# Kernel optimization log

Hardware: AMD Instinct MI355X
Metric: run time of the kernel (lower is better)

## Reference

```python
import jax, jax.numpy as jnp
import numpy as np

B, L, D, H, V = 4, 128, 128, 8, 32000
N_ITER = 4
DAMP_H = DAMP_Z = DAMP_X = 0.0
STEP_H = STEP_Z = STEP_X = 1.0
REG_H = REG_Z = REG_X = 1.0
BLOCK_MSG = False
NEG = 1e9


def _norm(t):
    # norm='softmax'
    return jax.nn.softmax(t, axis=-1)


def setup_inputs() -> dict:
    key = jax.random.key(0)
    k1, k2, k3, k4 = jax.random.split(key, 4)
    x = jax.random.normal(k1, (B, L, D), dtype=jnp.float32)
    mask = jnp.ones((B, L), dtype=jnp.int32)
    m_mask = jax.random.randint(k2, (B, L), 0, 2).astype(jnp.int32)
    embed_matrix = jax.random.normal(k3, (V, D), dtype=jnp.float32)
    ternary = jax.random.normal(k4, (2, D, D, H), dtype=jnp.float32)  # dists='' -> 2 groups
    return {"x": x, "mask": mask, "embed_matrix": embed_matrix, "m_mask": m_mask, "ternary": ternary}


def _forward(x, mask, embed_matrix, m_mask, ternary):
    dt = x.dtype
    mask1d = mask != 0                                   # [B,L] True = real token
    valid2d = mask1d[:, :, None] & mask1d[:, None, :]    # [B,L,L]
    inv2d = ~valid2d[:, None, :, :]                      # broadcast over heads
    keep = mask1d[..., None].astype(dt)                  # [B,L,1]
    mm = m_mask.astype(dt)[..., None]                    # [B,L,1]

    # distance mask: dists='' -> [triu(1); tril(-1)] -> [2,L,L]
    dm = jnp.triu(jnp.ones((L, L), dt), 1)
    distmask = jnp.stack([dm, dm.T], axis=0)

    eye = jnp.eye(L, dtype=dt)

    unary = x
    q_x = jnp.ones((B, L, V), dt)
    # initialize_Z=True: masked positions start from expected embedding
    pre = _norm(q_x) @ embed_matrix                      # [B,L,D]
    q_z = unary * (1.0 - mm) + pre * mm
    q_z = q_z * keep

    q_h = jnp.ones((B, H, L, L), dt) - eye * NEG
    q_h = jnp.where(inv2d, -NEG, q_h)

    cache_qh, cache_qz, cache_qx = q_h, q_z, q_x
    # async_update=True: normalize Z before first H update
    q_z = _norm(q_z) * keep

    for _ in range(N_ITER):
        # ---- H update: F[z,c,i,j] = sum_{k,a,b} q_z[z,i,a] q_z[z,j,b] T[k,a,b,c] dist[k,i,j]
        t1 = jnp.einsum('zia,kabc->zkibc', q_z, ternary)            # [B,2,L,D,H]
        F = jnp.einsum('zkibc,zjb,kij->zcij', t1, q_z, distmask)    # [B,H,L,L]
        q_h = cache_qh * DAMP_H + F * (1.0 - DAMP_H) / REG_H
        q_h = cache_qh * (1.0 - STEP_H) + q_h * STEP_H
        cache_qh = q_h
        q_h = q_h - eye * NEG
        q_h = jnp.where(inv2d, -NEG, q_h)
        q_hn = _norm(q_h)                                           # [B,H,L,L]

        # ---- Z update: first-order messages from ternary factors
        m = q_hn[:, None] * distmask[None, :, None]                 # [B,2,H,L,L]
        s1 = jnp.einsum('zkcij,zjb->zkibc', m, q_z)                 # to Z_i (head slot)
        G = jnp.einsum('zkibc,kabc->zia', s1, ternary)
        if not BLOCK_MSG:
            s2 = jnp.einsum('zkcij,zia->zkjac', m, q_z)             # to Z_j (dep slot)
            G = G + jnp.einsum('zkjac,kabc->zjb', s2, ternary)

        # unary: X message replaces word unary at <MASK> positions
        unary_eff = unary * (1.0 - mm) + (_norm(q_x) @ embed_matrix) * mm
        q_z_new = cache_qz * DAMP_Z + (unary_eff + G) * (1.0 - DAMP_Z) / REG_Z
        q_z_new = cache_qz * (1.0 - STEP_Z) + q_z_new * STEP_Z
        cache_qz = q_z_new
        q_z = _norm(q_z_new) * keep

        # ---- X update: message from Z through embedding factor
        msg_x = jnp.einsum('zia,va->ziv', q_z, embed_matrix)        # [B,L,V]
        q_x_new = cache_qx * DAMP_X + msg_x * (1.0 - DAMP_X) / REG_X
        q_x_new = cache_qx * (1.0 - STEP_X) + q_x_new * STEP_X
        cache_qx = q_x_new
        q_x = q_x_new

    # output_prob=False -> unnormalized scores
    return q_x


def reference(x, mask, embed_matrix, m_mask, ternary):
    return _forward(x, mask, embed_matrix, m_mask, ternary)
```

## Files before the change

### kernel.cpp

```cpp
#include <hip/hip_runtime.h>
#include <math.h>

#define L_ 128
#define D_ 128
#define H_ 8
#define V_ 32000
#define NEGC 1e9f

typedef short short8 __attribute__((ext_vector_type(8)));
typedef float f32x4 __attribute__((ext_vector_type(4)));
typedef unsigned short ushort8v __attribute__((ext_vector_type(8)));

__device__ __forceinline__ unsigned short f2bf(float x) {
    unsigned int u = __float_as_uint(x);
    unsigned int r = (u + 0x7fff + ((u >> 16) & 1)) >> 16;
    return (unsigned short)r;
}


__global__ __launch_bounds__(256) void prep_k(const float* __restrict__ E,
                                              unsigned short* __restrict__ Ebf,
                                              unsigned short* __restrict__ Etf,
                                              const float* __restrict__ T, float* __restrict__ Tt,
                                              const int* __restrict__ m_mask,
                                              int* __restrict__ rowidx, int* __restrict__ nactb,
                                              float* __restrict__ meansum) {
    __shared__ __align__(16) unsigned char psmem[8704];
    int blk = blockIdx.x;
    int t = threadIdx.x;
    if (blk < 1000) {
        unsigned short* tile = (unsigned short*)psmem;
        int v0 = blk * 32;
#pragma unroll
        for (int i = 0; i < 4; ++i) {
            int idx = i * 256 + t;
            int v = idx >> 5;
            int d4 = (idx & 31) * 4;
            float4 val = *(const float4*)&E[(size_t)(v0 + v) * 128 + d4];
            tile[v * 136 + d4 + 0] = f2bf(val.x);
            tile[v * 136 + d4 + 1] = f2bf(val.y);
            tile[v * 136 + d4 + 2] = f2bf(val.z);
            tile[v * 136 + d4 + 3] = f2bf(val.w);
        }
        __syncthreads();
        {
            int fi = t >> 5;
            int l0 = (t & 31) * 2;
            int vtl = fi >> 2, s = fi & 3;
            size_t base = ((size_t)(blk * 2 + vtl) * 4 + s) * 512;
#pragma unroll
            for (int li = 0; li < 2; ++li) {
                int l = l0 + li;
                int nl = l & 15, hf = l >> 4;
                ushort8v o;
#pragma unroll
                for (int j = 0; j < 8; ++j) o[j] = tile[(vtl * 16 + nl) * 136 + s * 32 + hf * 8 + j];
                *(ushort8v*)&Ebf[base + l * 8] = o;
            }
        }
        {
            int ct = t >> 5;
            int l0 = (t & 31) * 2;
            size_t base = ((size_t)blk * 8 + ct) * 512;
#pragma unroll
            for (int li = 0; li < 2; ++li) {
                int l = l0 + li;
                int nl = l & 15, hf = l >> 4;
                ushort8v o;
#pragma unroll
                for (int j = 0; j < 8; ++j) o[j] = tile[(hf * 8 + j) * 136 + ct * 16 + nl];
                *(ushort8v*)&Etf[base + l * 8] = o;
            }
        }
    } else if (blk < 1256) {
        int tb = blk - 1000;
        for (int q = 0; q < 4; ++q) {
            int id = tb * 1024 + q * 256 + t;
            int k = id >> 17;
            int rem = id & 131071;
            int a = rem >> 10;
            int bc = rem & 1023;
            int b = bc >> 3, c = bc & 7;
            Tt[k * 131072 + b * 1024 + a * 8 + c] = T[id];
        }
    } else if (blk == 1256) {
        int* wc = (int*)psmem;
        bool a0 = m_mask[t] != 0;
        bool a1 = m_mask[t + 256] != 0;
        unsigned long long b0 = __ballot(a0);
        unsigned long long b1 = __ballot(a1);
        int w = t >> 6, lane = t & 63;
        if (lane == 0) { wc[w] = __popcll(b0); wc[4 + w] = __popcll(b1); }
        __syncthreads();
        int base0 = 0;
        for (int i = 0; i < w; ++i) base0 += wc[i];
        int base1 = 0;
        for (int i = 0; i < 4 + w; ++i) base1 += wc[i];
        if (a0) rowidx[base0 + __popcll(b0 & ((1ull << lane) - 1))] = t;
        if (a1) rowidx[base1 + __popcll(b1 & ((1ull << lane) - 1))] = t + 256;
        if (t == 0) {
            int tot = 0;
            for (int i = 0; i < 8; ++i) tot += wc[i];
            nactb[0] = tot;
        }
    } else {
        float* red = (float*)psmem;
        int d = t & 127, h = t >> 7;
        int v0 = (blk - 1257) * 256;
        float s = 0.f;
        for (int p = 0; p < 128; ++p)
            s += E[(size_t)(v0 + h + 2 * p) * 128 + d];
        red[t] = s;
        __syncthreads();
        if (h == 0) atomicAdd(&meansum[d], red[d] + red[128 + d]);
    }
}

__global__ __launch_bounds__(64) void init_k(const float* __restrict__ x, const int* __restrict__ mask,
                                             const int* __restrict__ m_mask, const float* __restrict__ meansum,
                                             float* __restrict__ ue, float* __restrict__ qz,
                                             unsigned short* __restrict__ qzb) {
    int row = blockIdx.x, t = threadIdx.x;
    float keepv = mask[row] ? 1.f : 0.f;
    bool mm = m_mask[row] != 0;
    float pre0 = meansum[t] * (1.f / 32000.f);
    float pre1 = meansum[t + 64] * (1.f / 32000.f);
    float u0 = mm ? pre0 : x[row * 128 + t];
    float u1 = mm ? pre1 : x[row * 128 + t + 64];
    ue[row * 128 + t] = u0;
    ue[row * 128 + t + 64] = u1;
    float sv0 = u0 * keepv, sv1 = u1 * keepv;
    float m = fmaxf(sv0, sv1);
    for (int off = 32; off; off >>= 1) m = fmaxf(m, __shfl_xor(m, off));
    float e0 = __expf(sv0 - m), e1 = __expf(sv1 - m);
    float s = e0 + e1;
    for (int off = 32; off; off >>= 1) s += __shfl_xor(s, off);
    float inv = keepv / s;
    float q0 = e0 * inv, q1 = e1 * inv;
    qz[row * 128 + t] = q0;
    qz[row * 128 + t + 64] = q1;
    qzb[row * 128 + t] = f2bf(q0);
    qzb[row * 128 + t + 64] = f2bf(q1);
}


__global__ __launch_bounds__(256) void fusedA_k(const float* __restrict__ qz, const float* __restrict__ T,
                                                const float* __restrict__ Tt, float* __restrict__ U2,
                                                unsigned short* __restrict__ Ut, unsigned short* __restrict__ Wt,
                                                const unsigned short* __restrict__ qzb,
                                                const unsigned short* __restrict__ Ebf,
                                                const unsigned short* __restrict__ Etf,
                                                const int* __restrict__ rowidx, const int* __restrict__ nactb,
                                                float* __restrict__ partial, float* __restrict__ partial_rs) {
    __shared__ __align__(16) unsigned char smem[42752];
    int blk = blockIdx.x;
    int t = threadIdx.x;
    if (blk < 512) {
        float* aL = (float*)smem;
        int by = blk >> 5;
        int uw = by >> 3, z = (by >> 1) & 3, k = by & 1;
        int bx = blk & 31;
        int m0 = (bx >> 2) * 16, n = (bx & 3) * 256 + t;
        const float* A = qz + z * 16384;
        const float* Bm = (uw ? Tt : T) + k * 131072;
        for (int idx = t; idx < 2048; idx += 256)
            aL[idx] = A[(m0 + (idx >> 7)) * 128 + (idx & 127)];
        __syncthreads();
        float acc[16];
#pragma unroll
        for (int m = 0; m < 16; ++m) acc[m] = 0.f;
        for (int kq = 0; kq < 32; ++kq) {
            float b0 = Bm[(kq * 4 + 0) * 1024 + n];
            float b1 = Bm[(kq * 4 + 1) * 1024 + n];
            float b2 = Bm[(kq * 4 + 2) * 1024 + n];
            float b3 = Bm[(kq * 4 + 3) * 1024 + n];
#pragma unroll
            for (int m = 0; m < 16; ++m) {
                const float4 aq = *(const float4*)&aL[m * 128 + kq * 4];
                acc[m] += aq.x * b0 + aq.y * b1 + aq.z * b2 + aq.w * b3;
            }
        }
        if (uw == 0) {
            float* Cm = U2 + (z * 2 + k) * 131072;
#pragma unroll
            for (int m = 0; m < 16; ++m)
                Cm[(m0 + m) * 1024 + n] = acc[m];
        }
        int bb = n >> 3, cc = n & 7;
        ushort8v p0, p1;
#pragma unroll
        for (int m = 0; m < 8; ++m) { p0[m] = f2bf(acc[m]); p1[m] = f2bf(acc[8 + m]); }
        unsigned short* To = (uw ? Wt : Ut) + ((size_t)(z * 2 + k) * 128 + bb) * 1024 + cc * 128 + m0;
        *(ushort8v*)&To[0] = p0;
        *(ushort8v*)&To[8] = p1;
    } else {
        int nact = nactb[0];
        int bid = blk - 512;
        int xcd = bid & 7, idx = bid >> 3;
        int g = xcd + 8 * (idx >> 5);
        int bx = idx & 31;
        int r0 = bx * 16;
        if (g >= 50 || r0 >= nact) return;
        unsigned short* Pl = (unsigned short*)smem;
        float* slab = (float*)(smem + 9216);
        float* rsW  = (float*)(smem + 9216 + 33280);
        int w = t >> 6, lane = t & 63;
        int nloc = lane & 15, half = lane >> 4;
        int rA = r0 + nloc;
        bool actA = rA < nact;
        int rowA = actA ? rowidx[rA] : 0;
        short8 zero8 = (short8){0, 0, 0, 0, 0, 0, 0, 0};
        short8 afr[4];
#pragma unroll
        for (int s = 0; s < 4; ++s) {
            short8 v = *(const short8*)&qzb[rowA * 128 + s * 32 + half * 8];
            afr[s] = actA ? v : zero8;
        }
        const int kc0 = g * 20 + w * 5;
        short8 ebb[2][8];
#pragma unroll
        for (int f = 0; f < 8; ++f)
            ebb[0][f] = *(const short8*)&Ebf[((size_t)(kc0 * 8 + f)) * 512 + lane * 8];
        f32x4 acc2[8];
#pragma unroll
        for (int ct = 0; ct < 8; ++ct) acc2[ct] = (f32x4){0.f, 0.f, 0.f, 0.f};
        float rsl = 0.f;
#pragma unroll
        for (int step = 0; step < 5; ++step) {
            const int p = step & 1;
            const int kc = kc0 + step;
            short8 et[8];
#pragma unroll
            for (int f = 0; f < 8; ++f)
                et[f] = *(const short8*)&Etf[((size_t)(kc * 8 + f)) * 512 + lane * 8];
            if (step < 4) {
#pragma unroll
                for (int f = 0; f < 8; ++f)
                    ebb[p ^ 1][f] = *(const short8*)&Ebf[((size_t)((kc + 1) * 8 + f)) * 512 + lane * 8];
            }
            f32x4 p0 = (f32x4){0.f, 0.f, 0.f, 0.f};
            f32x4 p1 = (f32x4){0.f, 0.f, 0.f, 0.f};
#pragma unroll
            for (int s = 0; s < 4; ++s) {
                p0 = __builtin_amdgcn_mfma_f32_16x16x32_bf16(ebb[p][s], afr[s], p0, 0, 0, 0);
                p1 = __builtin_amdgcn_mfma_f32_16x16x32_bf16(ebb[p][4 + s], afr[s], p1, 0, 0, 0);
            }
            unsigned short* pw = Pl + (w * 2 + p) * 576;
            {
                float e0 = __expf(p0[0]), e1 = __expf(p0[1]), e2 = __expf(p0[2]), e3 = __expf(p0[3]);
                rsl += (e0 + e1) + (e2 + e3);
                uint2 pk = {(unsigned)f2bf(e0) | ((unsigned)f2bf(e1) << 16),
                            (unsigned)f2bf(e2) | ((unsigned)f2bf(e3) << 16)};
                *(uint2*)&pw[nloc * 36 + half * 4] = pk;
            }
            {
                float e0 = __expf(p1[0]), e1 = __expf(p1[1]), e2 = __expf(p1[2]), e3 = __expf(p1[3]);
                rsl += (e0 + e1) + (e2 + e3);
                uint2 pk = {(unsigned)f2bf(e0) | ((unsigned)f2bf(e1) << 16),
                            (unsigned)f2bf(e2) | ((unsigned)f2bf(e3) << 16)};
                *(uint2*)&pw[nloc * 36 + 16 + half * 4] = pk;
            }
            short8 a2 = *(const short8*)&pw[nloc * 36 + half * 8];
#pragma unroll
            for (int ct = 0; ct < 8; ++ct)
                acc2[ct] = __builtin_amdgcn_mfma_f32_16x16x32_bf16(a2, et[ct], acc2[ct], 0, 0, 0);
        }
        rsl += __shfl_xor(rsl, 16);
        rsl += __shfl_xor(rsl, 32);
        if (lane < 16) rsW[w * 16 + nloc] = rsl;
#pragma unroll
        for (int ct = 0; ct < 8; ++ct)
#pragma unroll
            for (int reg = 0; reg < 4; ++reg)
                slab[w * 2080 + (half * 4 + reg) * 130 + ct * 16 + nloc] = acc2[ct][reg];
        __syncthreads();
        float* pb = partial + (size_t)g * 65536;
        for (int i = t; i < 2048; i += 256) {
            int row = i >> 7, col = i & 127;
            int rr = r0 + row;
            if (rr < nact)
                pb[rr * 128 + col] = slab[row * 130 + col] + slab[2080 + row * 130 + col]
                                   + slab[4160 + row * 130 + col] + slab[6240 + row * 130 + col];
        }
        if (t < 16) {
            int rr = r0 + t;
            if (rr < nact)
                partial_rs[g * 512 + rr] = rsW[t] + rsW[16 + t] + rsW[32 + t] + rsW[48 + t];
        }
    }
}

__global__ __launch_bounds__(256) void fusedB_k(const float* __restrict__ qz, const float* __restrict__ U2,
                                                const int* __restrict__ mask,
                                                unsigned short* __restrict__ A0b, unsigned short* __restrict__ A1b,
                                                unsigned short* __restrict__ A0Tb, unsigned short* __restrict__ A1Tb,
                                                const float* __restrict__ partial, const float* __restrict__ partial_rs,
                                                const int* __restrict__ rowidx, const int* __restrict__ nactb,
                                                float* __restrict__ exbuf, float* __restrict__ rowsum) {
    __shared__ __align__(16) unsigned char smem[23552];
    int blk = blockIdx.x;
    int t = threadIdx.x;
    if (blk >= 256) {
        int nact = nactb[0];
        int idx = (blk - 256) * 256 + t;
        int rr = idx >> 7, col = idx & 127;
        if (rr >= nact) return;
        float s = 0.f;
#pragma unroll 10
        for (int g = 0; g < 50; ++g)
            s += partial[(size_t)g * 65536 + rr * 128 + col];
        int row = rowidx[rr];
        exbuf[row * 128 + col] = s;
        if (col == 0) {
            float ts = 0.f;
#pragma unroll 10
            for (int g = 0; g < 50; ++g) ts += partial_rs[g * 512 + rr];
            rowsum[row] = ts;
        }
        return;
    }
    float* As = (float*)smem;
    float* Bs = (float*)(smem + 4608);
    int* maskL = (int*)(smem + 4608 + 18432);
    int z = blk >> 6, c = (blk >> 3) & 7, iq = blk & 7;
    int i0 = iq * 16;
    int tj = t & 15, ti = t >> 4;
    int i = i0 + ti;
    if (t < 128) maskL[t] = mask[z * 128 + t];
    float acc0[8], acc1[8];
#pragma unroll
    for (int jj = 0; jj < 8; ++jj) { acc0[jj] = 0.f; acc1[jj] = 0.f; }
    const float* U2z = U2 + (size_t)z * 262144;
    const float* qzz = qz + z * 16384;
    for (int kb = 0; kb < 4; ++kb) {
        int b0 = kb * 32;
        __syncthreads();
        for (int e = t; e < 1024; e += 256) {
            int k = e >> 9, r = e & 511, ii = r >> 5, b = r & 31;
            As[(k * 16 + ii) * 36 + b] = U2z[k * 131072 + (i0 + ii) * 1024 + (b0 + b) * 8 + c];
        }
        for (int f = t; f < 1024; f += 256) {
            int j = f >> 3, b4 = f & 7;
            int slot = b4 ^ ((j >> 3) & 7);
            *(float4*)&Bs[j * 36 + slot * 4] = *(const float4*)&qzz[j * 128 + b0 + b4 * 4];
        }
        __syncthreads();
#pragma unroll
        for (int b4 = 0; b4 < 8; ++b4) {
            float4 a0 = *(const float4*)&As[(0 * 16 + ti) * 36 + b4 * 4];
            float4 a1 = *(const float4*)&As[(1 * 16 + ti) * 36 + b4 * 4];
#pragma unroll
            for (int jj = 0; jj < 8; ++jj) {
                int j = tj * 8 + jj;
                int slot = b4 ^ ((j >> 3) & 7);
                float4 bq = *(const float4*)&Bs[j * 36 + slot * 4];
                acc0[jj] += a0.x * bq.x;
                acc0[jj] += a0.y * bq.y;
                acc0[jj] += a0.z * bq.z;
                acc0[jj] += a0.w * bq.w;
                acc1[jj] += a1.x * bq.x;
                acc1[jj] += a1.y * bq.y;
                acc1[jj] += a1.z * bq.z;
                acc1[jj] += a1.w * bq.w;
            }
        }
    }
    bool vi = maskL[i] != 0;
    float fv[8];
#pragma unroll
    for (int jj = 0; jj < 8; ++jj) {
        int j2 = tj * 8 + jj;
        float F = (j2 > i) ? acc0[jj] : acc1[jj];
        if (j2 == i) F -= NEGC;
        if (!vi || maskL[j2] == 0) F = -NEGC;
        fv[jj] = F;
    }
    float mval = fv[0];
#pragma unroll
    for (int jj = 1; jj < 8; ++jj) mval = fmaxf(mval, fv[jj]);
    for (int off = 1; off < 16; off <<= 1) mval = fmaxf(mval, __shfl_xor(mval, off));
    float ssum = 0.f;
#pragma unroll
    for (int jj = 0; jj < 8; ++jj) ssum += __expf(fv[jj] - mval);
    for (int off = 1; off < 16; off <<= 1) ssum += __shfl_xor(ssum, off);
    float inv = 1.f / ssum;
    size_t base = (size_t)(z * 8 + c) * 16384;
    ushort8v v0, v1;
    unsigned short bvv[8];
#pragma unroll
    for (int jj = 0; jj < 8; ++jj) {
        int j2 = tj * 8 + jj;
        float val = __expf(fv[jj] - mval) * inv;
        unsigned short bv = f2bf(val);
        bvv[jj] = bv;
        v0[jj] = (j2 > i) ? bv : (unsigned short)0;
        v1[jj] = (j2 < i) ? bv : (unsigned short)0;
    }
    *(ushort8v*)&A0b[base + i * 128 + tj * 8] = v0;
    *(ushort8v*)&A1b[base + i * 128 + tj * 8] = v1;
#pragma unroll
    for (int jj = 0; jj < 8; ++jj) {
        int j2 = tj * 8 + jj;
        A0Tb[base + j2 * 128 + i] = (i < j2) ? bvv[jj] : (unsigned short)0;
        A1Tb[base + j2 * 128 + i] = (i > j2) ? bvv[jj] : (unsigned short)0;
    }
}

__global__ __launch_bounds__(64) void gkern_mfma_k(const unsigned short* __restrict__ A0b,
                                                   const unsigned short* __restrict__ A1b,
                                                   const unsigned short* __restrict__ A0Tb,
                                                   const unsigned short* __restrict__ A1Tb,
                                                   const unsigned short* __restrict__ Ut,
                                                   const unsigned short* __restrict__ Wt,
                                                   float* __restrict__ g1, float* __restrict__ g2) {
    int mode = blockIdx.y;
    int bx = blockIdx.x;
    int z = bx >> 6, it = (bx >> 3) & 7, at = bx & 7;
    int lane = threadIdx.x;
    int nloc = lane & 15, half = lane >> 4;
    int i0 = it * 16, a0 = at * 16;
    const unsigned short* Am0 = (mode ? A0Tb : A0b) + (size_t)z * 131072;
    const unsigned short* Am1 = (mode ? A1Tb : A1b) + (size_t)z * 131072;
    const unsigned short* Bt = mode ? Ut : Wt;
    const unsigned short* B0 = Bt + (size_t)(z * 2 + 0) * 131072 + (size_t)(a0 + nloc) * 1024;
    const unsigned short* B1 = Bt + (size_t)(z * 2 + 1) * 131072 + (size_t)(a0 + nloc) * 1024;
    const unsigned short* Ar0 = Am0 + (size_t)(i0 + nloc) * 128;
    const unsigned short* Ar1 = Am1 + (size_t)(i0 + nloc) * 128;
    f32x4 acc = (f32x4){0.f, 0.f, 0.f, 0.f};
#pragma unroll
    for (int c = 0; c < 8; ++c) {
#pragma unroll
        for (int sb = 0; sb < 4; ++sb) {
            int s0 = sb * 32 + half * 8;
            short8 av0 = *(const short8*)&Ar0[c * 16384 + s0];
            short8 bv0 = *(const short8*)&B0[c * 128 + s0];
            acc = __builtin_amdgcn_mfma_f32_16x16x32_bf16(av0, bv0, acc, 0, 0, 0);
            short8 av1 = *(const short8*)&Ar1[c * 16384 + s0];
            short8 bv1 = *(const short8*)&B1[c * 128 + s0];
            acc = __builtin_amdgcn_mfma_f32_16x16x32_bf16(av1, bv1, acc, 0, 0, 0);
        }
    }
    float* G = mode ? g2 : g1;
#pragma unroll
    for (int reg = 0; reg < 4; ++reg)
        G[(z * 128 + i0 + half * 4 + reg) * 128 + a0 + nloc] = acc[reg];
}

__global__ __launch_bounds__(64) void zupd_k(const float* __restrict__ ue, const float* __restrict__ x,
                                             const int* __restrict__ m_mask,
                                             const float* __restrict__ exbuf, const float* __restrict__ rowsum,
                                             const float* __restrict__ g1, const float* __restrict__ g2,
                                             const int* __restrict__ mask,
                                             float* __restrict__ qz, unsigned short* __restrict__ qzb, int useEx) {
    int row = blockIdx.x, t = threadIdx.x;
    float keepv = mask[row] ? 1.f : 0.f;
    int b = row * 128;
    float u0, u1;
    if (useEx) {
        if (m_mask[row] != 0) {
            float rsv = rowsum[row];
            u0 = exbuf[b + t] / rsv;
            u1 = exbuf[b + t + 64] / rsv;
        } else {
            u0 = x[b + t];
            u1 = x[b + t + 64];
        }
    } else {
        u0 = ue[b + t];
        u1 = ue[b + t + 64];
    }
    float v0 = u0 + g1[b + t] + g2[b + t];
    float v1 = u1 + g1[b + t + 64] + g2[b + t + 64];
    float m = fmaxf(v0, v1);
    for (int off = 32; off; off >>= 1) m = fmaxf(m, __shfl_xor(m, off));
    float e0 = __expf(v0 - m), e1 = __expf(v1 - m);
    float s = e0 + e1;
    for (int off = 32; off; off >>= 1) s += __shfl_xor(s, off);
    float inv = keepv / s;
    float q0 = e0 * inv, q1 = e1 * inv;
    qz[b + t] = q0;
    qz[b + t + 64] = q1;
    qzb[b + t] = f2bf(q0);
    qzb[b + t + 64] = f2bf(q1);
}

__global__ __launch_bounds__(256) void msgx_mfma_k(const unsigned short* __restrict__ qzb,
                                                   const unsigned short* __restrict__ Ebf,
                                                   float* __restrict__ out) {
    int t = threadIdx.x;
    int w = t >> 6, lane = t & 63;
    int nloc = lane & 15, half = lane >> 4;
    int rt0 = blockIdx.x * 64;
    int cb0 = blockIdx.y * 256 + w * 64;
    short8 afr[4][4];
#pragma unroll
    for (int r = 0; r < 4; ++r)
#pragma unroll
        for (int s = 0; s < 4; ++s)
            afr[r][s] = *(const short8*)&qzb[(rt0 + r * 16 + nloc) * 128 + s * 32 + half * 8];
    f32x4 acc[4][4];
#pragma unroll
    for (int r = 0; r < 4; ++r)
#pragma unroll
        for (int ct = 0; ct < 4; ++ct)
            acc[r][ct] = (f32x4){0.f, 0.f, 0.f, 0.f};
#pragma unroll
    for (int ct = 0; ct < 4; ++ct) {
#pragma unroll
        for (int s = 0; s < 4; ++s) {
            short8 bfr = *(const short8*)&Ebf[(((size_t)(cb0 >> 4) + ct) * 4 + s) * 512 + lane * 8];
#pragma unroll
            for (int r = 0; r < 4; ++r)
                acc[r][ct] = __builtin_amdgcn_mfma_f32_16x16x32_bf16(afr[r][s], bfr, acc[r][ct], 0, 0, 0);
        }
    }
#pragma unroll
    for (int r = 0; r < 4; ++r)
#pragma unroll
        for (int ct = 0; ct < 4; ++ct) {
            int col = cb0 + ct * 16 + nloc;
#pragma unroll
            for (int reg = 0; reg < 4; ++reg) {
                int row = rt0 + r * 16 + half * 4 + reg;
                out[(size_t)row * V_ + col] = acc[r][ct][reg];
            }
        }
}

extern "C" void kernel_launch(void* const* d_in, const int* in_sizes, int n_in,
                              void* d_out, int out_size, void* d_ws, size_t ws_size,
                              hipStream_t stream) {
    const float* x     = (const float*)d_in[0];
    const int*   mask  = (const int*)d_in[1];
    const float* E     = (const float*)d_in[2];
    const int*   mmask = (const int*)d_in[3];
    const float* T     = (const float*)d_in[4];
    float* out = (float*)d_out;

    float* w = (float*)d_ws;
    float* meansum = w;
    float* ue      = w + 128;
    float* qz      = ue + 65536;
    float* exbuf   = qz + 65536;
    float* rowsum  = exbuf + 65536;
    float* g1      = rowsum + 512;
    float* g2      = g1 + 65536;
    float* Tt      = g2 + 65536;
    float* U2      = Tt + 262144;
    float* prs     = U2 + 1048576;
    unsigned short* qzb  = (unsigned short*)(prs + 25600);
    unsigned short* Ebf  = qzb + 65536;
    unsigned short* Etf  = Ebf + 4096000;
    unsigned short* A0b  = Etf + 4096000;
    unsigned short* A1b  = A0b + 524288;
    unsigned short* A0Tb = A1b + 524288;
    unsigned short* A1Tb = A0Tb + 524288;
    unsigned short* Ut   = A1Tb + 524288;
    unsigned short* Wt   = Ut + 1048576;
    int* rowidx = (int*)(Wt + 1048576);
    int* nactb  = rowidx + 512;

    float* partial = out;

    hipMemsetAsync(meansum, 0, 128 * sizeof(float), stream);
    prep_k<<<1382, 256, 0, stream>>>(E, Ebf, Etf, T, Tt, mmask, rowidx, nactb, meansum);
    init_k<<<512, 64, 0, stream>>>(x, mask, mmask, meansum, ue, qz, qzb);

    for (int it = 0; it < 4; ++it) {
        fusedA_k<<<it ? 2304 : 512, 256, 0, stream>>>(qz, T, Tt, U2, Ut, Wt,
                                                      qzb, Ebf, Etf, rowidx, nactb, partial, prs);
        fusedB_k<<<it ? 512 : 256, 256, 0, stream>>>(qz, U2, mask, A0b, A1b, A0Tb, A1Tb,
                                                     partial, prs, rowidx, nactb, exbuf, rowsum);
        gkern_mfma_k<<<dim3(256, 2), 64, 0, stream>>>(A0b, A1b, A0Tb, A1Tb, Ut, Wt, g1, g2);
        zupd_k<<<512, 64, 0, stream>>>(ue, x, mmask, exbuf, rowsum, g1, g2, mask, qz, qzb, it ? 1 : 0);
    }
    msgx_mfma_k<<<dim3(8, 125), 256, 0, stream>>>(qzb, Ebf, out);
}
```

Before: 377.3 us.

## Fuse iteration loop into one persistent cooperative kernel with grid syncs

Replaces the 17 per-iteration kernel launches (four stages per iteration plus the final vocab projection) with one cooperative persistent kernel of 512 blocks. The blocks loop over the job lists and separate stages with grid.sync(). The goal is to remove launch overhead and inter-kernel gaps across the many small stages. In exchange, large stages such as the 2304-job pxe pass and the 1000-job msgx pass now run with a fixed 512-block grid, and each grid barrier has its own cost. A fallback path with separate launches remains for when the cooperative launch fails.

```diff
diff --git a/kernel.cpp b/kernel.cpp
--- a/kernel.cpp
+++ b/kernel.cpp
@@ -1,5 +1,8 @@
 #include <hip/hip_runtime.h>
+#include <hip/hip_cooperative_groups.h>
 #include <math.h>
+
+namespace cg = cooperative_groups;
 
 #define L_ 128
 #define D_ 128
@@ -16,6 +19,35 @@
     unsigned int r = (u + 0x7fff + ((u >> 16) & 1)) >> 16;
     return (unsigned short)r;
 }
+
+struct LoopArgs {
+    float* qz;
+    float* ue;
+    float* exbuf;
+    float* rowsum;
+    float* g1;
+    float* g2;
+    const float* x;
+    const float* T;
+    const float* Tt;
+    float* U2;
+    float* prs;
+    unsigned short* qzb;
+    const unsigned short* Ebf;
+    const unsigned short* Etf;
+    unsigned short* A0b;
+    unsigned short* A1b;
+    unsigned short* A0Tb;
+    unsigned short* A1Tb;
+    unsigned short* Ut;
+    unsigned short* Wt;
+    const int* mask;
+    const int* m_mask;
+    const int* rowidx;
+    const int* nactb;
+    float* partial;
+    float* out;
+};
 
 
 __global__ __launch_bounds__(256) void prep_k(const float* __restrict__ E,
@@ -144,181 +176,142 @@
 }
 
 
-__global__ __launch_bounds__(256) void fusedA_k(const float* __restrict__ qz, const float* __restrict__ T,
-                                                const float* __restrict__ Tt, float* __restrict__ U2,
-                                                unsigned short* __restrict__ Ut, unsigned short* __restrict__ Wt,
-                                                const unsigned short* __restrict__ qzb,
-                                                const unsigned short* __restrict__ Ebf,
-                                                const unsigned short* __restrict__ Etf,
-                                                const int* __restrict__ rowidx, const int* __restrict__ nactb,
-                                                float* __restrict__ partial, float* __restrict__ partial_rs) {
-    __shared__ __align__(16) unsigned char smem[42752];
-    int blk = blockIdx.x;
-    int t = threadIdx.x;
-    if (blk < 512) {
-        float* aL = (float*)smem;
-        int by = blk >> 5;
-        int uw = by >> 3, z = (by >> 1) & 3, k = by & 1;
-        int bx = blk & 31;
-        int m0 = (bx >> 2) * 16, n = (bx & 3) * 256 + t;
-        const float* A = qz + z * 16384;
-        const float* Bm = (uw ? Tt : T) + k * 131072;
-        for (int idx = t; idx < 2048; idx += 256)
-            aL[idx] = A[(m0 + (idx >> 7)) * 128 + (idx & 127)];
-        __syncthreads();
-        float acc[16];
-#pragma unroll
-        for (int m = 0; m < 16; ++m) acc[m] = 0.f;
-        for (int kq = 0; kq < 32; ++kq) {
-            float b0 = Bm[(kq * 4 + 0) * 1024 + n];
-            float b1 = Bm[(kq * 4 + 1) * 1024 + n];
-            float b2 = Bm[(kq * 4 + 2) * 1024 + n];
-            float b3 = Bm[(kq * 4 + 3) * 1024 + n];
-#pragma unroll
-            for (int m = 0; m < 16; ++m) {
-                const float4 aq = *(const float4*)&aL[m * 128 + kq * 4];
-                acc[m] += aq.x * b0 + aq.y * b1 + aq.z * b2 + aq.w * b3;
-            }
-        }
-        if (uw == 0) {
-            float* Cm = U2 + (z * 2 + k) * 131072;
-#pragma unroll
-            for (int m = 0; m < 16; ++m)
-                Cm[(m0 + m) * 1024 + n] = acc[m];
-        }
-        int bb = n >> 3, cc = n & 7;
-        ushort8v p0, p1;
-#pragma unroll
-        for (int m = 0; m < 8; ++m) { p0[m] = f2bf(acc[m]); p1[m] = f2bf(acc[8 + m]); }
-        unsigned short* To = (uw ? Wt : Ut) + ((size_t)(z * 2 + k) * 128 + bb) * 1024 + cc * 128 + m0;
-        *(ushort8v*)&To[0] = p0;
-        *(ushort8v*)&To[8] = p1;
-    } else {
-        int nact = nactb[0];
-        int bid = blk - 512;
-        int xcd = bid & 7, idx = bid >> 3;
-        int g = xcd + 8 * (idx >> 5);
-        int bx = idx & 31;
-        int r0 = bx * 16;
-        if (g >= 50 || r0 >= nact) return;
-        unsigned short* Pl = (unsigned short*)smem;
-        float* slab = (float*)(smem + 9216);
-        float* rsW  = (float*)(smem + 9216 + 33280);
-        int w = t >> 6, lane = t & 63;
-        int nloc = lane & 15, half = lane >> 4;
-        int rA = r0 + nloc;
-        bool actA = rA < nact;
-        int rowA = actA ? rowidx[rA] : 0;
-        short8 zero8 = (short8){0, 0, 0, 0, 0, 0, 0, 0};
-        short8 afr[4];
+__device__ __forceinline__ void dev_uwgemm(int blk, int t, unsigned char* smem, const LoopArgs& a) {
+    float* aL = (float*)smem;
+    int by = blk >> 5;
+    int uw = by >> 3, z = (by >> 1) & 3, k = by & 1;
+    int bx = blk & 31;
+    int m0 = (bx >> 2) * 16, n = (bx & 3) * 256 + t;
+    const float* A = a.qz + z * 16384;
+    const float* Bm = (uw ? a.Tt : a.T) + k * 131072;
+    for (int idx = t; idx < 2048; idx += 256)
+        aL[idx] = A[(m0 + (idx >> 7)) * 128 + (idx & 127)];
+    __syncthreads();
+    float acc[16];
+#pragma unroll
+    for (int m = 0; m < 16; ++m) acc[m] = 0.f;
+    for (int kq = 0; kq < 32; ++kq) {
+        float b0 = Bm[(kq * 4 + 0) * 1024 + n];
+        float b1 = Bm[(kq * 4 + 1) * 1024 + n];
+        float b2 = Bm[(kq * 4 + 2) * 1024 + n];
+        float b3 = Bm[(kq * 4 + 3) * 1024 + n];
+#pragma unroll
+        for (int m = 0; m < 16; ++m) {
+            const float4 aq = *(const float4*)&aL[m * 128 + kq * 4];
+            acc[m] += aq.x * b0 + aq.y * b1 + aq.z * b2 + aq.w * b3;
+        }
+    }
+    if (uw == 0) {
+        float* Cm = a.U2 + (z * 2 + k) * 131072;
+#pragma unroll
+        for (int m = 0; m < 16; ++m)
+            Cm[(m0 + m) * 1024 + n] = acc[m];
+    }
+    int bb = n >> 3, cc = n & 7;
+    ushort8v p0, p1;
+#pragma unroll
+    for (int m = 0; m < 8; ++m) { p0[m] = f2bf(acc[m]); p1[m] = f2bf(acc[8 + m]); }
+    unsigned short* To = (uw ? a.Wt : a.Ut) + ((size_t)(z * 2 + k) * 128 + bb) * 1024 + cc * 128 + m0;
+    *(ushort8v*)&To[0] = p0;
+    *(ushort8v*)&To[8] = p1;
+}
+
+__device__ __forceinline__ void dev_pxe(int bid, int t, unsigned char* smem, const LoopArgs& a) {
+    int nact = a.nactb[0];
+    int xcd = bid & 7, idx = bid >> 3;
+    int g = xcd + 8 * (idx >> 5);
+    int bx = idx & 31;
+    int r0 = bx * 16;
+    if (g >= 50 || r0 >= nact) return;
+    unsigned short* Pl = (unsigned short*)smem;
+    float* slab = (float*)(smem + 9216);
+    float* rsW  = (float*)(smem + 9216 + 33280);
+    int w = t >> 6, lane = t & 63;
+    int nloc = lane & 15, half = lane >> 4;
+    int rA = r0 + nloc;
+    bool actA = rA < nact;
+    int rowA = actA ? a.rowidx[rA] : 0;
+    short8 zero8 = (short8){0, 0, 0, 0, 0, 0, 0, 0};
+    short8 afr[4];
+#pragma unroll
+    for (int s = 0; s < 4; ++s) {
+        short8 v = *(const short8*)&a.qzb[rowA * 128 + s * 32 + half * 8];
+        afr[s] = actA ? v : zero8;
+    }
+    const int kc0 = g * 20 + w * 5;
+    short8 ebb[2][8];
+#pragma unroll
+    for (int f = 0; f < 8; ++f)
+        ebb[0][f] = *(const short8*)&a.Ebf[((size_t)(kc0 * 8 + f)) * 512 + lane * 8];
+    f32x4 acc2[8];
+#pragma unroll
+    for (int ct = 0; ct < 8; ++ct) acc2[ct] = (f32x4){0.f, 0.f, 0.f, 0.f};
+    float rsl = 0.f;
+#pragma unroll
+    for (int step = 0; step < 5; ++step) {
+        const int p = step & 1;
+        const int kc = kc0 + step;
+        short8 et[8];
+#pragma unroll
+        for (int f = 0; f < 8; ++f)
+            et[f] = *(const short8*)&a.Etf[((size_t)(kc * 8 + f)) * 512 + lane * 8];
+        if (step < 4) {
+#pragma unroll
+            for (int f = 0; f < 8; ++f)
+                ebb[p ^ 1][f] = *(const short8*)&a.Ebf[((size_t)((kc + 1) * 8 + f)) * 512 + lane * 8];
+        }
+        f32x4 p0 = (f32x4){0.f, 0.f, 0.f, 0.f};
+        f32x4 p1 = (f32x4){0.f, 0.f, 0.f, 0.f};
 #pragma unroll
         for (int s = 0; s < 4; ++s) {
-            short8 v = *(const short8*)&qzb[rowA * 128 + s * 32 + half * 8];
-            afr[s] = actA ? v : zero8;
-        }
-        const int kc0 = g * 20 + w * 5;
-        short8 ebb[2][8];
-#pragma unroll
-        for (int f = 0; f < 8; ++f)
-            ebb[0][f] = *(const short8*)&Ebf[((size_t)(kc0 * 8 + f)) * 512 + lane * 8];
-        f32x4 acc2[8];
-#pragma unroll
-        for (int ct = 0; ct < 8; ++ct) acc2[ct] = (f32x4){0.f, 0.f, 0.f, 0.f};
-        float rsl = 0.f;
-#pragma unroll
-        for (int step = 0; step < 5; ++step) {
-            const int p = step & 1;
-            const int kc = kc0 + step;
-            short8 et[8];
-#pragma unroll
-            for (int f = 0; f < 8; ++f)
-                et[f] = *(const short8*)&Etf[((size_t)(kc * 8 + f)) * 512 + lane * 8];
-            if (step < 4) {
-#pragma unroll
-                for (int f = 0; f < 8; ++f)
-                    ebb[p ^ 1][f] = *(const short8*)&Ebf[((size_t)((kc + 1) * 8 + f)) * 512 + lane * 8];
-            }
-            f32x4 p0 = (f32x4){0.f, 0.f, 0.f, 0.f};
-            f32x4 p1 = (f32x4){0.f, 0.f, 0.f, 0.f};
-#pragma unroll
-            for (int s = 0; s < 4; ++s) {
-                p0 = __builtin_amdgcn_mfma_f32_16x16x32_bf16(ebb[p][s], afr[s], p0, 0, 0, 0);
-                p1 = __builtin_amdgcn_mfma_f32_16x16x32_bf16(ebb[p][4 + s], afr[s], p1, 0, 0, 0);
-            }
-            unsigned short* pw = Pl + (w * 2 + p) * 576;
-            {
-                float e0 = __expf(p0[0]), e1 = __expf(p0[1]), e2 = __expf(p0[2]), e3 = __expf(p0[3]);
-                rsl += (e0 + e1) + (e2 + e3);
-                uint2 pk = {(unsigned)f2bf(e0) | ((unsigned)f2bf(e1) << 16),
-                            (unsigned)f2bf(e2) | ((unsigned)f2bf(e3) << 16)};
-                *(uint2*)&pw[nloc * 36 + half * 4] = pk;
-            }
-            {
-                float e0 = __expf(p1[0]), e1 = __expf(p1[1]), e2 = __expf(p1[2]), e3 = __expf(p1[3]);
-                rsl += (e0 + e1) + (e2 + e3);
-                uint2 pk = {(unsigned)f2bf(e0) | ((unsigned)f2bf(e1) << 16),
-                            (unsigned)f2bf(e2) | ((unsigned)f2bf(e3) << 16)};
-                *(uint2*)&pw[nloc * 36 + 16 + half * 4] = pk;
-            }
-            short8 a2 = *(const short8*)&pw[nloc * 36 + half * 8];
-#pragma unroll
-            for (int ct = 0; ct < 8; ++ct)
-                acc2[ct] = __builtin_amdgcn_mfma_f32_16x16x32_bf16(a2, et[ct], acc2[ct], 0, 0, 0);
-        }
-        rsl += __shfl_xor(rsl, 16);
-        rsl += __shfl_xor(rsl, 32);
-        if (lane < 16) rsW[w * 16 + nloc] = rsl;
+            p0 = __builtin_amdgcn_mfma_f32_16x16x32_bf16(ebb[p][s], afr[s], p0, 0, 0, 0);
+            p1 = __builtin_amdgcn_mfma_f32_16x16x32_bf16(ebb[p][4 + s], afr[s], p1, 0, 0, 0);
+        }
+        unsigned short* pw = Pl + (w * 2 + p) * 576;
+        {
+            float e0 = __expf(p0[0]), e1 = __expf(p0[1]), e2 = __expf(p0[2]), e3 = __expf(p0[3]);
+            rsl += (e0 + e1) + (e2 + e3);
+            uint2 pk = {(unsigned)f2bf(e0) | ((unsigned)f2bf(e1) << 16),
+                        (unsigned)f2bf(e2) | ((unsigned)f2bf(e3) << 16)};
+            *(uint2*)&pw[nloc * 36 + half * 4] = pk;
+        }
+        {
+            float e0 = __expf(p1[0]), e1 = __expf(p1[1]), e2 = __expf(p1[2]), e3 = __expf(p1[3]);
+            rsl += (e0 + e1) + (e2 + e3);
+            uint2 pk = {(unsigned)f2bf(e0) | ((unsigned)f2bf(e1) << 16),
+                        (unsigned)f2bf(e2) | ((unsigned)f2bf(e3) << 16)};
+            *(uint2*)&pw[nloc * 36 + 16 + half * 4] = pk;
+        }
+        short8 a2 = *(const short8*)&pw[nloc * 36 + half * 8];
 #pragma unroll
         for (int ct = 0; ct < 8; ++ct)
-#pragma unroll
-            for (int reg = 0; reg < 4; ++reg)
-                slab[w * 2080 + (half * 4 + reg) * 130 + ct * 16 + nloc] = acc2[ct][reg];
-        __syncthreads();
-        float* pb = partial + (size_t)g * 65536;
-        for (int i = t; i < 2048; i += 256) {
-            int row = i >> 7, col = i & 127;
-            int rr = r0 + row;
-            if (rr < nact)
-                pb[rr * 128 + col] = slab[row * 130 + col] + slab[2080 + row * 130 + col]
-                                   + slab[4160 + row * 130 + col] + slab[6240 + row * 130 + col];
-        }
-        if (t < 16) {
-            int rr = r0 + t;
-            if (rr < nact)
-                partial_rs[g * 512 + rr] = rsW[t] + rsW[16 + t] + rsW[32 + t] + rsW[48 + t];
-        }
-    }
-}
-
-__global__ __launch_bounds__(256) void fusedB_k(const float* __restrict__ qz, const float* __restrict__ U2,
-                                                const int* __restrict__ mask,
-                                                unsigned short* __restrict__ A0b, unsigned short* __restrict__ A1b,
-                                                unsigned short* __restrict__ A0Tb, unsigned short* __restrict__ A1Tb,
-                                                const float* __restrict__ partial, const float* __restrict__ partial_rs,
-                                                const int* __restrict__ rowidx, const int* __restrict__ nactb,
-                                                float* __restrict__ exbuf, float* __restrict__ rowsum) {
-    __shared__ __align__(16) unsigned char smem[23552];
-    int blk = blockIdx.x;
-    int t = threadIdx.x;
-    if (blk >= 256) {
-        int nact = nactb[0];
-        int idx = (blk - 256) * 256 + t;
-        int rr = idx >> 7, col = idx & 127;
-        if (rr >= nact) return;
-        float s = 0.f;
-#pragma unroll 10
-        for (int g = 0; g < 50; ++g)
-            s += partial[(size_t)g * 65536 + rr * 128 + col];
-        int row = rowidx[rr];
-        exbuf[row * 128 + col] = s;
-        if (col == 0) {
-            float ts = 0.f;
-#pragma unroll 10
-            for (int g = 0; g < 50; ++g) ts += partial_rs[g * 512 + rr];
-            rowsum[row] = ts;
-        }
-        return;
-    }
+            acc2[ct] = __builtin_amdgcn_mfma_f32_16x16x32_bf16(a2, et[ct], acc2[ct], 0, 0, 0);
+    }
+    rsl += __shfl_xor(rsl, 16);
+    rsl += __shfl_xor(rsl, 32);
+    if (lane < 16) rsW[w * 16 + nloc] = rsl;
+#pragma unroll
+    for (int ct = 0; ct < 8; ++ct)
+#pragma unroll
+        for (int reg = 0; reg < 4; ++reg)
+            slab[w * 2080 + (half * 4 + reg) * 130 + ct * 16 + nloc] = acc2[ct][reg];
+    __syncthreads();
+    float* pb = a.partial + (size_t)g * 65536;
+    for (int i = t; i < 2048; i += 256) {
+        int row = i >> 7, col = i & 127;
+        int rr = r0 + row;
+        if (rr < nact)
+            pb[rr * 128 + col] = slab[row * 130 + col] + slab[2080 + row * 130 + col]
+                               + slab[4160 + row * 130 + col] + slab[6240 + row * 130 + col];
+    }
+    if (t < 16) {
+        int rr = r0 + t;
+        if (rr < nact)
+            a.prs[g * 512 + rr] = rsW[t] + rsW[16 + t] + rsW[32 + t] + rsW[48 + t];
+    }
+}
+
+__device__ __forceinline__ void dev_qhnF(int blk, int t, unsigned char* smem, const LoopArgs& a) {
     float* As = (float*)smem;
     float* Bs = (float*)(smem + 4608);
     int* maskL = (int*)(smem + 4608 + 18432);
@@ -326,12 +319,12 @@
     int i0 = iq * 16;
     int tj = t & 15, ti = t >> 4;
     int i = i0 + ti;
-    if (t < 128) maskL[t] = mask[z * 128 + t];
+    if (t < 128) maskL[t] = a.mask[z * 128 + t];
     float acc0[8], acc1[8];
 #pragma unroll
     for (int jj = 0; jj < 8; ++jj) { acc0[jj] = 0.f; acc1[jj] = 0.f; }
-    const float* U2z = U2 + (size_t)z * 262144;
-    const float* qzz = qz + z * 16384;
+    const float* U2z = a.U2 + (size_t)z * 262144;
+    const float* qzz = a.qz + z * 16384;
     for (int kb = 0; kb < 4; ++kb) {
         int b0 = kb * 32;
         __syncthreads();
@@ -396,32 +389,44 @@
         v0[jj] = (j2 > i) ? bv : (unsigned short)0;
         v1[jj] = (j2 < i) ? bv : (unsigned short)0;
     }
-    *(ushort8v*)&A0b[base + i * 128 + tj * 8] = v0;
-    *(ushort8v*)&A1b[base + i * 128 + tj * 8] = v1;
+    *(ushort8v*)&a.A0b[base + i * 128 + tj * 8] = v0;
+    *(ushort8v*)&a.A1b[base + i * 128 + tj * 8] = v1;
 #pragma unroll
     for (int jj = 0; jj < 8; ++jj) {
         int j2 = tj * 8 + jj;
-        A0Tb[base + j2 * 128 + i] = (i < j2) ? bvv[jj] : (unsigned short)0;
-        A1Tb[base + j2 * 128 + i] = (i > j2) ? bvv[jj] : (unsigned short)0;
-    }
-}
-
-__global__ __launch_bounds__(64) void gkern_mfma_k(const unsigned short* __restrict__ A0b,
-                                                   const unsigned short* __restrict__ A1b,
-                                                   const unsigned short* __restrict__ A0Tb,
-                                                   const unsigned short* __restrict__ A1Tb,
-                                                   const unsigned short* __restrict__ Ut,
-                                                   const unsigned short* __restrict__ Wt,
-                                                   float* __restrict__ g1, float* __restrict__ g2) {
-    int mode = blockIdx.y;
-    int bx = blockIdx.x;
+        a.A0Tb[base + j2 * 128 + i] = (i < j2) ? bvv[jj] : (unsigned short)0;
+        a.A1Tb[base + j2 * 128 + i] = (i > j2) ? bvv[jj] : (unsigned short)0;
+    }
+}
+
+__device__ __forceinline__ void dev_reduce(int blk, int t, const LoopArgs& a) {
+    int nact = a.nactb[0];
+    int idx = blk * 256 + t;
+    int rr = idx >> 7, col = idx & 127;
+    if (rr >= nact) return;
+    float s = 0.f;
+#pragma unroll 10
+    for (int g = 0; g < 50; ++g)
+        s += a.partial[(size_t)g * 65536 + rr * 128 + col];
+    int row = a.rowidx[rr];
+    a.exbuf[row * 128 + col] = s;
+    if (col == 0) {
+        float ts = 0.f;
+#pragma unroll 10
+        for (int g = 0; g < 50; ++g) ts += a.prs[g * 512 + rr];
+        a.rowsum[row] = ts;
+    }
+}
+
+__device__ __forceinline__ void dev_gkern(int unit, int lane, const LoopArgs& a) {
+    int mode = unit >> 8;
+    int bx = unit & 255;
     int z = bx >> 6, it = (bx >> 3) & 7, at = bx & 7;
-    int lane = threadIdx.x;
     int nloc = lane & 15, half = lane >> 4;
     int i0 = it * 16, a0 = at * 16;
-    const unsigned short* Am0 = (mode ? A0Tb : A0b) + (size_t)z * 131072;
-    const unsigned short* Am1 = (mode ? A1Tb : A1b) + (size_t)z * 131072;
-    const unsigned short* Bt = mode ? Ut : Wt;
+    const unsigned short* Am0 = (mode ? a.A0Tb : a.A0b) + (size_t)z * 131072;
+    const unsigned short* Am1 = (mode ? a.A1Tb : a.A1b) + (size_t)z * 131072;
+    const unsigned short* Bt = mode ? a.Ut : a.Wt;
     const unsigned short* B0 = Bt + (size_t)(z * 2 + 0) * 131072 + (size_t)(a0 + nloc) * 1024;
     const unsigned short* B1 = Bt + (size_t)(z * 2 + 1) * 131072 + (size_t)(a0 + nloc) * 1024;
     const unsigned short* Ar0 = Am0 + (size_t)(i0 + nloc) * 128;
@@ -440,37 +445,31 @@
             acc = __builtin_amdgcn_mfma_f32_16x16x32_bf16(av1, bv1, acc, 0, 0, 0);
         }
     }
-    float* G = mode ? g2 : g1;
+    float* G = mode ? a.g2 : a.g1;
 #pragma unroll
     for (int reg = 0; reg < 4; ++reg)
         G[(z * 128 + i0 + half * 4 + reg) * 128 + a0 + nloc] = acc[reg];
 }
 
-__global__ __launch_bounds__(64) void zupd_k(const float* __restrict__ ue, const float* __restrict__ x,
-                                             const int* __restrict__ m_mask,
-                                             const float* __restrict__ exbuf, const float* __restrict__ rowsum,
-                                             const float* __restrict__ g1, const float* __restrict__ g2,
-                                             const int* __restrict__ mask,
-                                             float* __restrict__ qz, unsigned short* __restrict__ qzb, int useEx) {
-    int row = blockIdx.x, t = threadIdx.x;
-    float keepv = mask[row] ? 1.f : 0.f;
+__device__ __forceinline__ void dev_zupd(int row, int t, const LoopArgs& a, int useEx) {
+    float keepv = a.mask[row] ? 1.f : 0.f;
     int b = row * 128;
     float u0, u1;
     if (useEx) {
-        if (m_mask[row] != 0) {
-            float rsv = rowsum[row];
-            u0 = exbuf[b + t] / rsv;
-            u1 = exbuf[b + t + 64] / rsv;
+        if (a.m_mask[row] != 0) {
+            float rsv = a.rowsum[row];
+            u0 = a.exbuf[b + t] / rsv;
+            u1 = a.exbuf[b + t + 64] / rsv;
         } else {
-            u0 = x[b + t];
-            u1 = x[b + t + 64];
+            u0 = a.x[b + t];
+            u1 = a.x[b + t + 64];
         }
     } else {
-        u0 = ue[b + t];
-        u1 = ue[b + t + 64];
-    }
-    float v0 = u0 + g1[b + t] + g2[b + t];
-    float v1 = u1 + g1[b + t + 64] + g2[b + t + 64];
+        u0 = a.ue[b + t];
+        u1 = a.ue[b + t + 64];
+    }
+    float v0 = u0 + a.g1[b + t] + a.g2[b + t];
+    float v1 = u1 + a.g1[b + t + 64] + a.g2[b + t + 64];
     float m = fmaxf(v0, v1);
     for (int off = 32; off; off >>= 1) m = fmaxf(m, __shfl_xor(m, off));
     float e0 = __expf(v0 - m), e1 = __expf(v1 - m);
@@ -478,53 +477,115 @@
     for (int off = 32; off; off >>= 1) s += __shfl_xor(s, off);
     float inv = keepv / s;
     float q0 = e0 * inv, q1 = e1 * inv;
-    qz[b + t] = q0;
-    qz[b + t + 64] = q1;
-    qzb[b + t] = f2bf(q0);
-    qzb[b + t + 64] = f2bf(q1);
-}
-
-__global__ __launch_bounds__(256) void msgx_mfma_k(const unsigned short* __restrict__ qzb,
-                                                   const unsigned short* __restrict__ Ebf,
-                                                   float* __restrict__ out) {
+    a.qz[b + t] = q0;
+    a.qz[b + t + 64] = q1;
+    a.qzb[b + t] = f2bf(q0);
+    a.qzb[b + t + 64] = f2bf(q1);
+}
+
+__device__ __forceinline__ void dev_msgx(int job, int t, const LoopArgs& a) {
+    int w = t >> 6, lane = t & 63;
+    int nloc = lane & 15, half = lane >> 4;
+    int rt0 = (job & 7) * 64;
+    int cb0 = (job >> 3) * 256 + w * 64;
+    short8 afr[4][4];
+#pragma unroll
+    for (int r = 0; r < 4; ++r)
+#pragma unroll
+        for (int s = 0; s < 4; ++s)
+            afr[r][s] = *(const short8*)&a.qzb[(rt0 + r * 16 + nloc) * 128 + s * 32 + half * 8];
+    f32x4 acc[4][4];
+#pragma unroll
+    for (int r = 0; r < 4; ++r)
+#pragma unroll
+        for (int ct = 0; ct < 4; ++ct)
+            acc[r][ct] = (f32x4){0.f, 0.f, 0.f, 0.f};
+#pragma unroll
+    for (int ct = 0; ct < 4; ++ct) {
+#pragma unroll
+        for (int s = 0; s < 4; ++s) {
+            short8 bfr = *(const short8*)&a.Ebf[(((size_t)(cb0 >> 4) + ct) * 4 + s) * 512 + lane * 8];
+#pragma unroll
+            for (int r = 0; r < 4; ++r)
+                acc[r][ct] = __builtin_amdgcn_mfma_f32_16x16x32_bf16(afr[r][s], bfr, acc[r][ct], 0, 0, 0);
+        }
+    }
+#pragma unroll
+    for (int r = 0; r < 4; ++r)
+#pragma unroll
+        for (int ct = 0; ct < 4; ++ct) {
+            int col = cb0 + ct * 16 + nloc;
+#pragma unroll
+            for (int reg = 0; reg < 4; ++reg) {
+                int row = rt0 + r * 16 + half * 4 + reg;
+                a.out[(size_t)row * V_ + col] = acc[r][ct][reg];
+            }
+        }
+}
+
+__global__ __launch_bounds__(256, 2) void loop_k(LoopArgs a) {
+    cg::grid_group grid = cg::this_grid();
+    __shared__ __align__(16) unsigned char smem[42752];
     int t = threadIdx.x;
     int w = t >> 6, lane = t & 63;
-    int nloc = lane & 15, half = lane >> 4;
-    int rt0 = blockIdx.x * 64;
-    int cb0 = blockIdx.y * 256 + w * 64;
-    short8 afr[4][4];
-#pragma unroll
-    for (int r = 0; r < 4; ++r)
-#pragma unroll
-        for (int s = 0; s < 4; ++s)
-            afr[r][s] = *(const short8*)&qzb[(rt0 + r * 16 + nloc) * 128 + s * 32 + half * 8];
-    f32x4 acc[4][4];
-#pragma unroll
-    for (int r = 0; r < 4; ++r)
-#pragma unroll
-        for (int ct = 0; ct < 4; ++ct)
-            acc[r][ct] = (f32x4){0.f, 0.f, 0.f, 0.f};
-#pragma unroll
-    for (int ct = 0; ct < 4; ++ct) {
-#pragma unroll
-        for (int s = 0; s < 4; ++s) {
-            short8 bfr = *(const short8*)&Ebf[(((size_t)(cb0 >> 4) + ct) * 4 + s) * 512 + lane * 8];
-#pragma unroll
-            for (int r = 0; r < 4; ++r)
-                acc[r][ct] = __builtin_amdgcn_mfma_f32_16x16x32_bf16(afr[r][s], bfr, acc[r][ct], 0, 0, 0);
-        }
-    }
-#pragma unroll
-    for (int r = 0; r < 4; ++r)
-#pragma unroll
-        for (int ct = 0; ct < 4; ++ct) {
-            int col = cb0 + ct * 16 + nloc;
-#pragma unroll
-            for (int reg = 0; reg < 4; ++reg) {
-                int row = rt0 + r * 16 + half * 4 + reg;
-                out[(size_t)row * V_ + col] = acc[r][ct][reg];
-            }
-        }
+    const int G = gridDim.x;
+    for (int it = 0; it < 4; ++it) {
+        int nA = it ? 2304 : 512;
+        for (int job = blockIdx.x; job < nA; job += G) {
+            __syncthreads();
+            if (job < 512) dev_uwgemm(job, t, smem, a);
+            else dev_pxe(job - 512, t, smem, a);
+        }
+        grid.sync();
+        int nB = it ? 512 : 256;
+        for (int job = blockIdx.x; job < nB; job += G) {
+            __syncthreads();
+            if (job < 256) dev_qhnF(job, t, smem, a);
+            else dev_reduce(job - 256, t, a);
+        }
+        grid.sync();
+        for (int jb = blockIdx.x; jb < 128; jb += G)
+            dev_gkern(jb * 4 + w, lane, a);
+        grid.sync();
+        for (int jb = blockIdx.x; jb < 128; jb += G)
+            dev_zupd(jb * 4 + w, lane, a, it ? 1 : 0);
+        grid.sync();
+    }
+    for (int job = blockIdx.x; job < 1000; job += G)
+        dev_msgx(job, t, a);
+}
+
+__global__ __launch_bounds__(256) void fA_k(LoopArgs a, int it) {
+    __shared__ __align__(16) unsigned char smem[42752];
+    int nA = it ? 2304 : 512;
+    for (int job = blockIdx.x; job < nA; job += gridDim.x) {
+        __syncthreads();
+        if (job < 512) dev_uwgemm(job, threadIdx.x, smem, a);
+        else dev_pxe(job - 512, threadIdx.x, smem, a);
+    }
+}
+__global__ __launch_bounds__(256) void fB_k(LoopArgs a, int it) {
+    __shared__ __align__(16) unsigned char smem[42752];
+    int nB = it ? 512 : 256;
+    for (int job = blockIdx.x; job < nB; job += gridDim.x) {
+        __syncthreads();
+        if (job < 256) dev_qhnF(job, threadIdx.x, smem, a);
+        else dev_reduce(job - 256, threadIdx.x, a);
+    }
+}
+__global__ __launch_bounds__(256) void fG_k(LoopArgs a) {
+    int w = threadIdx.x >> 6, lane = threadIdx.x & 63;
+    for (int jb = blockIdx.x; jb < 128; jb += gridDim.x)
+        dev_gkern(jb * 4 + w, lane, a);
+}
+__global__ __launch_bounds__(256) void fZ_k(LoopArgs a, int it) {
+    int w = threadIdx.x >> 6, lane = threadIdx.x & 63;
+    for (int jb = blockIdx.x; jb < 128; jb += gridDim.x)
+        dev_zupd(jb * 4 + w, lane, a, it ? 1 : 0);
+}
+__global__ __launch_bounds__(256) void fM_k(LoopArgs a) {
+    for (int job = blockIdx.x; job < 1000; job += gridDim.x)
+        dev_msgx(job, threadIdx.x, a);
 }
 
 extern "C" void kernel_launch(void* const* d_in, const int* in_sizes, int n_in,
@@ -566,13 +627,24 @@
     prep_k<<<1382, 256, 0, stream>>>(E, Ebf, Etf, T, Tt, mmask, rowidx, nactb, meansum);
     init_k<<<512, 64, 0, stream>>>(x, mask, mmask, meansum, ue, qz, qzb);
 
-    for (int it = 0; it < 4; ++it) {
-        fusedA_k<<<it ? 2304 : 512, 256, 0, stream>>>(qz, T, Tt, U2, Ut, Wt,
-                                                      qzb, Ebf, Etf, rowidx, nactb, partial, prs);
-        fusedB_k<<<it ? 512 : 256, 256, 0, stream>>>(qz, U2, mask, A0b, A1b, A0Tb, A1Tb,
-                                                     partial, prs, rowidx, nactb, exbuf, rowsum);
-        gkern_mfma_k<<<dim3(256, 2), 64, 0, stream>>>(A0b, A1b, A0Tb, A1Tb, Ut, Wt, g1, g2);
-        zupd_k<<<512, 64, 0, stream>>>(ue, x, mmask, exbuf, rowsum, g1, g2, mask, qz, qzb, it ? 1 : 0);
-    }
-    msgx_mfma_k<<<dim3(8, 125), 256, 0, stream>>>(qzb, Ebf, out);
-}
+    LoopArgs args;
+    args.qz = qz; args.ue = ue; args.exbuf = exbuf; args.rowsum = rowsum;
+    args.g1 = g1; args.g2 = g2; args.x = x; args.T = T; args.Tt = Tt;
+    args.U2 = U2; args.prs = prs; args.qzb = qzb; args.Ebf = Ebf; args.Etf = Etf;
+    args.A0b = A0b; args.A1b = A1b; args.A0Tb = A0Tb; args.A1Tb = A1Tb;
+    args.Ut = Ut; args.Wt = Wt; args.mask = mask; args.m_mask = mmask;
+    args.rowidx = rowidx; args.nactb = nactb; args.partial = partial; args.out = out;
+
+    void* kp[] = { (void*)&args };
+    hipError_t err = hipLaunchCooperativeKernel((const void*)loop_k, dim3(512), dim3(256),
+                                                kp, 0, stream);
+    if (err != hipSuccess) {
+        for (int it = 0; it < 4; ++it) {
+            fA_k<<<it ? 2304 : 512, 256, 0, stream>>>(args, it);
+            fB_k<<<it ? 512 : 256, 256, 0, stream>>>(args, it);
+            fG_k<<<128, 256, 0, stream>>>(args);
+            fZ_k<<<128, 256, 0, stream>>>(args, it);
+        }
+        fM_k<<<1000, 256, 0, stream>>>(args);
+    }
+}
```

Result: slower. 1.404 ms (+272.0%).
